# Kernel tuning notes

Measured on AMD Instinct MI355X. Metric: run time of the kernel, lower is better.

The kernel has to match this reference:

```python
import jax, jax.numpy as jnp
import numpy as np

B, S, IN_DIM, OUT_DIM = 16, 1024, 1024, 1024
NEG_SLOPE = 0.01  # torch F.leaky_relu default


def setup_inputs() -> dict:
    key = jax.random.key(0)
    ks = jax.random.split(key, 10)
    sc_in = 1.0 / np.sqrt(IN_DIM)
    sc_out = 1.0 / np.sqrt(OUT_DIM)
    return {
        "xs": jax.random.normal(ks[0], (B, S, IN_DIM), dtype=jnp.float32),
        "mask": jax.random.randint(ks[1], (B, S), 0, 2, dtype=jnp.int32),
        "Wk": jax.random.uniform(ks[2], (OUT_DIM, IN_DIM), jnp.float32, -sc_in, sc_in),
        "bk": jax.random.uniform(ks[3], (OUT_DIM,), jnp.float32, -sc_in, sc_in),
        "Wq": jax.random.uniform(ks[4], (OUT_DIM, IN_DIM), jnp.float32, -sc_in, sc_in),
        "bq": jax.random.uniform(ks[5], (OUT_DIM,), jnp.float32, -sc_in, sc_in),
        "Wv": jax.random.uniform(ks[6], (OUT_DIM, IN_DIM), jnp.float32, -sc_in, sc_in),
        "bv": jax.random.uniform(ks[7], (OUT_DIM,), jnp.float32, -sc_in, sc_in),
        "Wlin": jax.random.uniform(ks[8], (OUT_DIM, OUT_DIM), jnp.float32, -sc_out, sc_out),
        "blin": jax.random.uniform(ks[9], (OUT_DIM,), jnp.float32, -sc_out, sc_out),
    }


def reference(xs, mask, Wk, bk, Wq, bq, Wv, bv, Wlin, blin):
    # projections: torch Linear is x @ W.T + b
    K = jnp.einsum('bsi,oi->bso', xs, Wk) + bk  # [B,S,D]
    Q = jnp.einsum('bsi,oi->bso', xs, Wq) + bq  # [B,S,D]
    V = jnp.einsum('bsi,oi->bso', xs, Wv) + bv  # [B,S,D]
    # qk[b,s,e] = sum_d K[b,s,d] * Q[b,e,d]
    qk = jnp.einsum('bsd,bed->bse', K, Q) / xs.shape[-1]
    # mask.repeat(1,S).view(B,S,S) => element [b,i,j] = mask[b,j] (column/key mask)
    qk = jnp.where(mask[:, None, :].astype(bool), qk, -jnp.inf)
    a = jax.nn.softmax(qk, axis=-1)  # [B,S,S]
    # faithful to einsum('bij,bik->bik'): sum a over last axis, scale V elementwise
    attn = jnp.sum(a, axis=-1, keepdims=True) * V  # [B,S,D]
    out = jnp.einsum('bsd,od->bso', attn, Wlin) + blin
    return jnp.where(out >= 0, out, NEG_SLOPE * out)
```

## Files before the change

kernel.cpp:

```cpp
#include <hip/hip_runtime.h>
#include <hip/hip_bf16.h>
#include <stdint.h>


#define M_TOT 16384
#define KDIM  1024
#define NDIM  1024
#define NT    32

typedef __attribute__((ext_vector_type(8))) short bf16x8;
typedef __attribute__((ext_vector_type(4))) float f32x4;
typedef __attribute__((ext_vector_type(4))) unsigned short u16x4;
typedef __attribute__((ext_vector_type(8))) unsigned short u16x8;

static __device__ __forceinline__ unsigned short f2bf(float f) {
    union { float f; unsigned int u; } v; v.f = f;
    unsigned int u = v.u;
    return (unsigned short)((u + 0x7fffu + ((u >> 16) & 1u)) >> 16);
}

static __device__ __forceinline__ void gload16(const void* g, void* l) {
    __builtin_amdgcn_global_load_lds(
        (__attribute__((address_space(1))) void*)(g),
        (__attribute__((address_space(3))) void*)(l), 16, 0, 0);
}

static __device__ __forceinline__ int swz(int p) {
    return p ^ (((p >> 9) & 1) << 5) ^ (((p >> 8) & 1) << 4);
}

__global__ __launch_bounds__(256) void prep_kernel(
    const float* __restrict__ xs, const float* __restrict__ Wv,
    const float* __restrict__ bv, const float* __restrict__ Wlin,
    const float* __restrict__ blin, unsigned short* __restrict__ Wc,
    float* __restrict__ bcomb, unsigned short* __restrict__ Xb) {
    __shared__ unsigned short Al[64 * 32];
    __shared__ unsigned short Bl[64 * 32];
    const int bid = blockIdx.x;
    const int t = threadIdx.x;

    if (bid < 256) {
        const int ot = bid >> 4;
        const int it = bid & 15;
        const int w = t >> 6, l = t & 63;
        const int wr = (w >> 1) * 32, wc = (w & 1) * 32;
        const int lr = l & 15, lk = l >> 4;

        f32x4 acc[2][2] = {};

        for (int kt = 0; kt < KDIM / 32; ++kt) {
            float4 av[2];
            #pragma unroll
            for (int j = 0; j < 2; ++j) {
                const int row = j * 32 + (t >> 3);
                const int kq = t & 7;
                av[j] = *(const float4*)&Wlin[(ot * 64 + row) * KDIM + kt * 32 + kq * 4];
            }
            float4 bvv[2];
            #pragma unroll
            for (int j = 0; j < 2; ++j) {
                const int d = j * 16 + (t >> 4);
                const int i4 = t & 15;
                bvv[j] = *(const float4*)&Wv[(kt * 32 + d) * NDIM + it * 64 + i4 * 4];
            }
            __syncthreads();
            #pragma unroll
            for (int j = 0; j < 2; ++j) {
                const int row = j * 32 + (t >> 3);
                const int kq = t & 7;
                u16x4 p = { f2bf(av[j].x), f2bf(av[j].y), f2bf(av[j].z), f2bf(av[j].w) };
                *(u16x4*)&Al[row * 32 + kq * 4] = p;
            }
            #pragma unroll
            for (int j = 0; j < 2; ++j) {
                const int d = j * 16 + (t >> 4);
                const int i4 = t & 15;
                Bl[(i4 * 4 + 0) * 32 + d] = f2bf(bvv[j].x);
                Bl[(i4 * 4 + 1) * 32 + d] = f2bf(bvv[j].y);
                Bl[(i4 * 4 + 2) * 32 + d] = f2bf(bvv[j].z);
                Bl[(i4 * 4 + 3) * 32 + d] = f2bf(bvv[j].w);
            }
            __syncthreads();
            bf16x8 af[2], bfr[2];
            #pragma unroll
            for (int fi = 0; fi < 2; ++fi)
                af[fi] = *(bf16x8*)&Al[(wr + fi * 16 + lr) * 32 + lk * 8];
            #pragma unroll
            for (int fj = 0; fj < 2; ++fj)
                bfr[fj] = *(bf16x8*)&Bl[(wc + fj * 16 + lr) * 32 + lk * 8];
            #pragma unroll
            for (int fi = 0; fi < 2; ++fi)
                #pragma unroll
                for (int fj = 0; fj < 2; ++fj)
                    acc[fi][fj] = __builtin_amdgcn_mfma_f32_16x16x32_bf16(
                        af[fi], bfr[fj], acc[fi][fj], 0, 0, 0);
            __syncthreads();
        }
        #pragma unroll
        for (int fi = 0; fi < 2; ++fi)
            #pragma unroll
            for (int fj = 0; fj < 2; ++fj)
                #pragma unroll
                for (int r = 0; r < 4; ++r) {
                    const int o = ot * 64 + wr + fi * 16 + lk * 4 + r;
                    const int i = it * 64 + wc + fj * 16 + lr;
                    Wc[o * KDIM + i] = f2bf(acc[fi][fj][r]);
                }
    } else if (bid < 512) {
        const int wave = t >> 6, lane = t & 63;
        const int o = (bid - 256) * 4 + wave;
        float s = 0.f;
        for (int d = lane; d < KDIM; d += 64) s += Wlin[o * KDIM + d] * bv[d];
        #pragma unroll
        for (int off = 32; off > 0; off >>= 1) s += __shfl_down(s, off, 64);
        if (lane == 0) bcomb[o] = s + blin[o];
    } else {
        const int cb = bid - 512;
        const size_t base = ((size_t)cb * 256 + t) * 8;
        #pragma unroll
        for (int itr = 0; itr < 4; ++itr) {
            const size_t idx = base + (size_t)itr * (size_t)(2048 * 256 * 8);
            float4 a = *(const float4*)&xs[idx];
            float4 b = *(const float4*)&xs[idx + 4];
            u16x8 p = { f2bf(a.x), f2bf(a.y), f2bf(a.z), f2bf(a.w),
                        f2bf(b.x), f2bf(b.y), f2bf(b.z), f2bf(b.w) };
            *(u16x8*)&Xb[idx] = p;
        }
    }
}

__global__ __launch_bounds__(512, 2) void main_gemm_8p(
    const unsigned short* __restrict__ Xb, const unsigned short* __restrict__ Wc,
    const float* __restrict__ bcomb, float* __restrict__ out) {
    extern __shared__ char lds[];
    const int tid = threadIdx.x;
    const int w = tid >> 6, l = tid & 63;
    const int wm = w >> 2, wn = w & 3;
    const int lr = l & 15, lk = l >> 4;

    const int swzb = ((blockIdx.x & 7) << 5) + (blockIdx.x >> 3);
    const int mt = swzb >> 2, nt = swzb & 3;

    int aoff[8], boff[4];
    #pragma unroll
    for (int fi = 0; fi < 8; ++fi)
        aoff[fi] = swz((wm * 128 + fi * 16 + lr) * 64 + lk * 16);
    #pragma unroll
    for (int fj = 0; fj < 4; ++fj)
        boff[fj] = 16384 + swz((wn * 64 + fj * 16 + lr) * 64 + lk * 16);

    const char* srcA0; const char* srcA1; const char* srcB0; const char* srcB1;
    {
        int q0 = 0 * 8192 + w * 1024 + l * 16, p0 = swz(q0);
        int q1 = 1 * 8192 + w * 1024 + l * 16, p1 = swz(q1);
        srcA0 = (const char*)Xb + ((size_t)(mt * 256 + (p0 >> 6)) * KDIM) * 2 + (p0 & 63);
        srcA1 = (const char*)Xb + ((size_t)(mt * 256 + (p1 >> 6)) * KDIM) * 2 + (p1 & 63);
        srcB0 = (const char*)Wc + ((size_t)(nt * 256 + (p0 >> 6)) * KDIM) * 2 + (p0 & 63);
        srcB1 = (const char*)Wc + ((size_t)(nt * 256 + (p1 >> 6)) * KDIM) * 2 + (p1 & 63);
    }
    const int ldsw = w * 1024;

    f32x4 acc[8][4] = {};

    #pragma unroll
    for (int pt = 0; pt < 3; ++pt) {
        char* bb = lds + pt * 32768;
        gload16(srcA0 + (size_t)pt * 64, bb + ldsw);
        gload16(srcA1 + (size_t)pt * 64, bb + 8192 + ldsw);
        gload16(srcB0 + (size_t)pt * 64, bb + 16384 + ldsw);
        gload16(srcB1 + (size_t)pt * 64, bb + 24576 + ldsw);
    }

#define KTILE(T, STAGE_EN)                                                     \
    do {                                                                       \
        const char* bufp = lds + (size_t)((T) & 3) * 32768;                    \
        char* nb = lds + (size_t)(((T) + 3) & 3) * 32768;                      \
               \
        if (STAGE_EN) {                                                        \
            gload16(srcA0 + (size_t)((T) + 3) * 64, nb + ldsw);                \
            gload16(srcA1 + (size_t)((T) + 3) * 64, nb + 8192 + ldsw);         \
        }                                                                      \
        bf16x8 bfr[4], afr[4];                                                 \
        _Pragma("unroll")                                                      \
        for (int fj = 0; fj < 4; ++fj)                                         \
            bfr[fj] = *(const bf16x8*)(bufp + boff[fj]);                       \
        _Pragma("unroll")                                                      \
        for (int fi = 0; fi < 4; ++fi)                                         \
            afr[fi] = *(const bf16x8*)(bufp + aoff[fi]);                       \
        __builtin_amdgcn_s_barrier();                                          \
        __builtin_amdgcn_s_setprio(1);                                         \
        _Pragma("unroll")                                                      \
        for (int fi = 0; fi < 4; ++fi)                                         \
            _Pragma("unroll")                                                  \
            for (int fj = 0; fj < 4; ++fj)                                     \
                acc[fi][fj] = __builtin_amdgcn_mfma_f32_16x16x32_bf16(         \
                    afr[fi], bfr[fj], acc[fi][fj], 0, 0, 0);                   \
        __builtin_amdgcn_s_setprio(0);                                         \
        __builtin_amdgcn_s_barrier();                                          \
                        \
        if (STAGE_EN) {                                                        \
            gload16(srcB0 + (size_t)((T) + 3) * 64, nb + 16384 + ldsw);        \
            gload16(srcB1 + (size_t)((T) + 3) * 64, nb + 24576 + ldsw);        \
        }                                                                      \
        bf16x8 af2[4];                                                         \
        _Pragma("unroll")                                                      \
        for (int fi = 0; fi < 4; ++fi)                                         \
            af2[fi] = *(const bf16x8*)(bufp + aoff[4 + fi]);                   \
        __builtin_amdgcn_s_barrier();                                          \
        __builtin_amdgcn_s_setprio(1);                                         \
        _Pragma("unroll")                                                      \
        for (int fi = 0; fi < 4; ++fi)                                         \
            _Pragma("unroll")                                                  \
            for (int fj = 0; fj < 4; ++fj)                                     \
                acc[4 + fi][fj] = __builtin_amdgcn_mfma_f32_16x16x32_bf16(     \
                    af2[fi], bfr[fj], acc[4 + fi][fj], 0, 0, 0);               \
        __builtin_amdgcn_s_setprio(0);                                         \
    } while (0)

    for (int t = 0; t < NT - 3; ++t) {
        asm volatile("s_waitcnt vmcnt(8)" ::: "memory");
        __builtin_amdgcn_s_barrier();
        KTILE(t, 1);
    }
    asm volatile("s_waitcnt vmcnt(8)" ::: "memory");
    __builtin_amdgcn_s_barrier();
    KTILE(29, 0);
    asm volatile("s_waitcnt vmcnt(4)" ::: "memory");
    __builtin_amdgcn_s_barrier();
    KTILE(30, 0);
    asm volatile("s_waitcnt vmcnt(0)" ::: "memory");
    __builtin_amdgcn_s_barrier();
    KTILE(31, 0);
#undef KTILE

    #pragma unroll
    for (int fi = 0; fi < 8; ++fi)
        #pragma unroll
        for (int fj = 0; fj < 4; ++fj) {
            const int col = nt * 256 + wn * 64 + fj * 16 + lr;
            const float b = bcomb[col];
            #pragma unroll
            for (int r = 0; r < 4; ++r) {
                const int row = mt * 256 + wm * 128 + fi * 16 + lk * 4 + r;
                float v = acc[fi][fj][r] + b;
                out[(size_t)row * NDIM + col] = v >= 0.f ? v : 0.01f * v;
            }
        }
}

__global__ __launch_bounds__(256) void main_gemm_f32(
    const float* __restrict__ X, const unsigned short* __restrict__ Wc,
    const float* __restrict__ bcomb, float* __restrict__ out) {
    __shared__ unsigned short As[128 * 32];
    __shared__ unsigned short Bs[128 * 32];
    const int t = threadIdx.x;
    const int nt = blockIdx.x & 7;
    const int mt = blockIdx.x >> 3;
    const int w = t >> 6, l = t & 63;
    const int wr = (w >> 1) * 64, wcc = (w & 1) * 64;
    const int lr = l & 15, lk = l >> 4;

    f32x4 acc[4][4] = {};

    const int arow = t >> 3;
    const int akq = t & 7;
    const int brow = t >> 2;
    const int bc4 = t & 3;

    for (int kt = 0; kt < KDIM / 32; ++kt) {
        float4 av[4];
        #pragma unroll
        for (int j = 0; j < 4; ++j) {
            const int row = j * 32 + arow;
            av[j] = *(const float4*)&X[(mt * 128 + row) * KDIM + kt * 32 + akq * 4];
        }
        __syncthreads();
        #pragma unroll
        for (int j = 0; j < 4; ++j) {
            const int row = j * 32 + arow;
            u16x4 p = { f2bf(av[j].x), f2bf(av[j].y), f2bf(av[j].z), f2bf(av[j].w) };
            *(u16x4*)&As[row * 32 + akq * 4] = p;
        }
        #pragma unroll
        for (int j = 0; j < 2; ++j) {
            const int row = j * 64 + brow;
            const unsigned short* g = &Wc[(nt * 128 + row) * KDIM + kt * 32 + bc4 * 8];
            unsigned short* ldst = &Bs[(j * 256 + w * 64) * 8];
            gload16(g, ldst);
        }
        __syncthreads();
        bf16x8 af[4], bfr[4];
        #pragma unroll
        for (int fi = 0; fi < 4; ++fi)
            af[fi] = *(bf16x8*)&As[(wr + fi * 16 + lr) * 32 + lk * 8];
        #pragma unroll
        for (int fj = 0; fj < 4; ++fj)
            bfr[fj] = *(bf16x8*)&Bs[(wcc + fj * 16 + lr) * 32 + lk * 8];
        #pragma unroll
        for (int fi = 0; fi < 4; ++fi)
            #pragma unroll
            for (int fj = 0; fj < 4; ++fj)
                acc[fi][fj] = __builtin_amdgcn_mfma_f32_16x16x32_bf16(
                    af[fi], bfr[fj], acc[fi][fj], 0, 0, 0);
    }

    #pragma unroll
    for (int fi = 0; fi < 4; ++fi)
        #pragma unroll
        for (int fj = 0; fj < 4; ++fj) {
            const int col = nt * 128 + wcc + fj * 16 + lr;
            const float b = bcomb[col];
            #pragma unroll
            for (int r = 0; r < 4; ++r) {
                const int row = mt * 128 + wr + fi * 16 + lk * 4 + r;
                float v = acc[fi][fj][r] + b;
                out[row * NDIM + col] = v >= 0.f ? v : 0.01f * v;
            }
        }
}

extern "C" void kernel_launch(void* const* d_in, const int* in_sizes, int n_in,
                              void* d_out, int out_size, void* d_ws, size_t ws_size,
                              hipStream_t stream) {
    const float* xs   = (const float*)d_in[0];
    const float* Wv   = (const float*)d_in[6];
    const float* bv   = (const float*)d_in[7];
    const float* Wlin = (const float*)d_in[8];
    const float* blin = (const float*)d_in[9];

    unsigned short* Wc = (unsigned short*)d_ws;
    float* bcomb = (float*)((char*)d_ws + 2097152);
    unsigned short* Xb = (unsigned short*)((char*)d_ws + 2101248);
    float* out = (float*)d_out;

    const size_t NEED = 2101248 + (size_t)M_TOT * KDIM * 2;
    if (ws_size >= NEED) {
        (void)hipFuncSetAttribute((const void*)main_gemm_8p,
                                  hipFuncAttributeMaxDynamicSharedMemorySize,
                                  131072);
        hipLaunchKernelGGL(prep_kernel, dim3(512 + 2048), dim3(256), 0, stream,
                           xs, Wv, bv, Wlin, blin, Wc, bcomb, Xb);
        hipLaunchKernelGGL(main_gemm_8p, dim3(256), dim3(512), 131072, stream,
                           Xb, Wc, bcomb, out);
    } else {
        hipLaunchKernelGGL(prep_kernel, dim3(512), dim3(256), 0, stream,
                           xs, Wv, bv, Wlin, blin, Wc, bcomb, Xb);
        hipLaunchKernelGGL(main_gemm_f32, dim3((M_TOT / 128) * (NDIM / 128)),
                           dim3(256), 0, stream, xs, Wc, bcomb, out);
    }
}
```

Measured before the change: 86.14 us.

## Split weight-fusion prep into bf16 convert/transpose pass and tiled MFMA GEMM

The Wlin·Wv combined-weight computation moves from a 256-block kernel that converted fp32 to bf16 inside its k-loop into two stages. The first kernel transposes Wv and converts Wv and Wlin to bf16 scratch buffers placed in the output buffer. The second runs a 64-block 128x128 MFMA GEMM using direct global-to-LDS loads, alongside the xs conversion blocks. This targets the long serial prep GEMM that held up the main kernel, at the cost of an extra launch and reusing the output buffer as scratch.

```diff
diff --git a/kernel.cpp b/kernel.cpp
--- a/kernel.cpp
+++ b/kernel.cpp
@@ -29,94 +29,75 @@
     return p ^ (((p >> 9) & 1) << 5) ^ (((p >> 8) & 1) << 4);
 }
 
-__global__ __launch_bounds__(256) void prep_kernel(
-    const float* __restrict__ xs, const float* __restrict__ Wv,
-    const float* __restrict__ bv, const float* __restrict__ Wlin,
-    const float* __restrict__ blin, unsigned short* __restrict__ Wc,
-    float* __restrict__ bcomb, unsigned short* __restrict__ Xb) {
-    __shared__ unsigned short Al[64 * 32];
-    __shared__ unsigned short Bl[64 * 32];
+__global__ __launch_bounds__(256) void prep0_kernel(
+    const float* __restrict__ Wv, const float* __restrict__ Wlin,
+    const float* __restrict__ bv, const float* __restrict__ blin,
+    unsigned short* __restrict__ Wvt, unsigned short* __restrict__ Wlb,
+    float* __restrict__ bcomb) {
+    __shared__ float Tl[64 * 65];
     const int bid = blockIdx.x;
     const int t = threadIdx.x;
 
     if (bid < 256) {
-        const int ot = bid >> 4;
+        const int dt = bid >> 4;
         const int it = bid & 15;
-        const int w = t >> 6, l = t & 63;
-        const int wr = (w >> 1) * 32, wc = (w & 1) * 32;
-        const int lr = l & 15, lk = l >> 4;
-
-        f32x4 acc[2][2] = {};
-
-        for (int kt = 0; kt < KDIM / 32; ++kt) {
-            float4 av[2];
-            #pragma unroll
-            for (int j = 0; j < 2; ++j) {
-                const int row = j * 32 + (t >> 3);
-                const int kq = t & 7;
-                av[j] = *(const float4*)&Wlin[(ot * 64 + row) * KDIM + kt * 32 + kq * 4];
-            }
-            float4 bvv[2];
-            #pragma unroll
-            for (int j = 0; j < 2; ++j) {
-                const int d = j * 16 + (t >> 4);
-                const int i4 = t & 15;
-                bvv[j] = *(const float4*)&Wv[(kt * 32 + d) * NDIM + it * 64 + i4 * 4];
-            }
-            __syncthreads();
-            #pragma unroll
-            for (int j = 0; j < 2; ++j) {
-                const int row = j * 32 + (t >> 3);
-                const int kq = t & 7;
-                u16x4 p = { f2bf(av[j].x), f2bf(av[j].y), f2bf(av[j].z), f2bf(av[j].w) };
-                *(u16x4*)&Al[row * 32 + kq * 4] = p;
-            }
-            #pragma unroll
-            for (int j = 0; j < 2; ++j) {
-                const int d = j * 16 + (t >> 4);
-                const int i4 = t & 15;
-                Bl[(i4 * 4 + 0) * 32 + d] = f2bf(bvv[j].x);
-                Bl[(i4 * 4 + 1) * 32 + d] = f2bf(bvv[j].y);
-                Bl[(i4 * 4 + 2) * 32 + d] = f2bf(bvv[j].z);
-                Bl[(i4 * 4 + 3) * 32 + d] = f2bf(bvv[j].w);
-            }
-            __syncthreads();
-            bf16x8 af[2], bfr[2];
-            #pragma unroll
-            for (int fi = 0; fi < 2; ++fi)
-                af[fi] = *(bf16x8*)&Al[(wr + fi * 16 + lr) * 32 + lk * 8];
-            #pragma unroll
-            for (int fj = 0; fj < 2; ++fj)
-                bfr[fj] = *(bf16x8*)&Bl[(wc + fj * 16 + lr) * 32 + lk * 8];
-            #pragma unroll
-            for (int fi = 0; fi < 2; ++fi)
-                #pragma unroll
-                for (int fj = 0; fj < 2; ++fj)
-                    acc[fi][fj] = __builtin_amdgcn_mfma_f32_16x16x32_bf16(
-                        af[fi], bfr[fj], acc[fi][fj], 0, 0, 0);
-            __syncthreads();
-        }
-        #pragma unroll
-        for (int fi = 0; fi < 2; ++fi)
-            #pragma unroll
-            for (int fj = 0; fj < 2; ++fj)
-                #pragma unroll
-                for (int r = 0; r < 4; ++r) {
-                    const int o = ot * 64 + wr + fi * 16 + lk * 4 + r;
-                    const int i = it * 64 + wc + fj * 16 + lr;
-                    Wc[o * KDIM + i] = f2bf(acc[fi][fj][r]);
-                }
+        const int r = t >> 2;
+        const int c0 = (t & 3) * 16;
+        #pragma unroll
+        for (int u = 0; u < 4; ++u) {
+            float4 v = *(const float4*)&Wv[((size_t)(dt * 64 + r)) * NDIM + it * 64 + c0 + 4 * u];
+            Tl[r * 65 + c0 + 4 * u + 0] = v.x;
+            Tl[r * 65 + c0 + 4 * u + 1] = v.y;
+            Tl[r * 65 + c0 + 4 * u + 2] = v.z;
+            Tl[r * 65 + c0 + 4 * u + 3] = v.w;
+        }
+        __syncthreads();
+        const int i = t >> 2;
+        const int dq = (t & 3) * 16;
+        float v[16];
+        #pragma unroll
+        for (int u = 0; u < 16; ++u) v[u] = Tl[(dq + u) * 65 + i];
+        u16x8 p0 = { f2bf(v[0]), f2bf(v[1]), f2bf(v[2]), f2bf(v[3]),
+                     f2bf(v[4]), f2bf(v[5]), f2bf(v[6]), f2bf(v[7]) };
+        u16x8 p1 = { f2bf(v[8]), f2bf(v[9]), f2bf(v[10]), f2bf(v[11]),
+                     f2bf(v[12]), f2bf(v[13]), f2bf(v[14]), f2bf(v[15]) };
+        unsigned short* dst = &Wvt[((size_t)(it * 64 + i)) * KDIM + dt * 64 + dq];
+        *(u16x8*)dst = p0;
+        *(u16x8*)(dst + 8) = p1;
     } else if (bid < 512) {
+        const size_t idx = (((size_t)(bid - 256)) * 256 + t) * 16;
+        float4 a = *(const float4*)&Wlin[idx];
+        float4 b = *(const float4*)&Wlin[idx + 4];
+        float4 c = *(const float4*)&Wlin[idx + 8];
+        float4 d = *(const float4*)&Wlin[idx + 12];
+        u16x8 p0 = { f2bf(a.x), f2bf(a.y), f2bf(a.z), f2bf(a.w),
+                     f2bf(b.x), f2bf(b.y), f2bf(b.z), f2bf(b.w) };
+        u16x8 p1 = { f2bf(c.x), f2bf(c.y), f2bf(c.z), f2bf(c.w),
+                     f2bf(d.x), f2bf(d.y), f2bf(d.z), f2bf(d.w) };
+        *(u16x8*)&Wlb[idx] = p0;
+        *(u16x8*)&Wlb[idx + 8] = p1;
+    } else {
         const int wave = t >> 6, lane = t & 63;
-        const int o = (bid - 256) * 4 + wave;
+        const int o = (bid - 512) * 4 + wave;
         float s = 0.f;
         for (int d = lane; d < KDIM; d += 64) s += Wlin[o * KDIM + d] * bv[d];
         #pragma unroll
         for (int off = 32; off > 0; off >>= 1) s += __shfl_down(s, off, 64);
         if (lane == 0) bcomb[o] = s + blin[o];
-    } else {
-        const int cb = bid - 512;
-        const size_t base = ((size_t)cb * 256 + t) * 8;
+    }
+}
+
+__global__ __launch_bounds__(256) void prep1_kernel(
+    const unsigned short* __restrict__ Wlb, const unsigned short* __restrict__ Wvt,
+    const float* __restrict__ xs, unsigned short* __restrict__ Wc,
+    unsigned short* __restrict__ Xb) {
+    __shared__ unsigned short As[128 * 32];
+    __shared__ unsigned short Bs[128 * 32];
+    const int bid = blockIdx.x;
+    const int t = threadIdx.x;
+
+    if (bid >= 64) {
+        const size_t base = (((size_t)(bid - 64)) * 256 + t) * 8;
         #pragma unroll
         for (int itr = 0; itr < 4; ++itr) {
             const size_t idx = base + (size_t)itr * (size_t)(2048 * 256 * 8);
@@ -126,7 +107,58 @@
                         f2bf(b.x), f2bf(b.y), f2bf(b.z), f2bf(b.w) };
             *(u16x8*)&Xb[idx] = p;
         }
-    }
+        return;
+    }
+
+    const int nt8 = bid & 7;
+    const int mt8 = bid >> 3;
+    const int w = t >> 6, l = t & 63;
+    const int wr = (w >> 1) * 64, wcc = (w & 1) * 64;
+    const int lr = l & 15, lk = l >> 4;
+
+    f32x4 acc[4][4] = {};
+
+    const int srow = t >> 2;
+    const int sc8 = (t & 3) * 8;
+    const unsigned short* gA = &Wlb[((size_t)(mt8 * 128) + srow) * KDIM + sc8];
+    const unsigned short* gB = &Wvt[((size_t)(nt8 * 128) + srow) * KDIM + sc8];
+    unsigned short* lA0 = &As[w * 512];
+    unsigned short* lB0 = &Bs[w * 512];
+
+    for (int kt = 0; kt < KDIM / 32; ++kt) {
+        #pragma unroll
+        for (int j = 0; j < 2; ++j) {
+            gload16(gA + (size_t)j * 64 * KDIM + kt * 32, lA0 + j * 2048);
+            gload16(gB + (size_t)j * 64 * KDIM + kt * 32, lB0 + j * 2048);
+        }
+        __syncthreads();
+        bf16x8 af[4], bfr[4];
+        #pragma unroll
+        for (int fi = 0; fi < 4; ++fi)
+            af[fi] = *(bf16x8*)&As[(wr + fi * 16 + lr) * 32 + lk * 8];
+        #pragma unroll
+        for (int fj = 0; fj < 4; ++fj)
+            bfr[fj] = *(bf16x8*)&Bs[(wcc + fj * 16 + lr) * 32 + lk * 8];
+        #pragma unroll
+        for (int fi = 0; fi < 4; ++fi)
+            #pragma unroll
+            for (int fj = 0; fj < 4; ++fj)
+                acc[fi][fj] = __builtin_amdgcn_mfma_f32_16x16x32_bf16(
+                    af[fi], bfr[fj], acc[fi][fj], 0, 0, 0);
+        __syncthreads();
+    }
+
+    #pragma unroll
+    for (int fi = 0; fi < 4; ++fi)
+        #pragma unroll
+        for (int fj = 0; fj < 4; ++fj) {
+            const int col = nt8 * 128 + wcc + fj * 16 + lr;
+            #pragma unroll
+            for (int r = 0; r < 4; ++r) {
+                const int row = mt8 * 128 + wr + fi * 16 + lk * 4 + r;
+                Wc[(size_t)row * KDIM + col] = f2bf(acc[fi][fj][r]);
+            }
+        }
 }
 
 __global__ __launch_bounds__(512, 2) void main_gemm_8p(
@@ -175,7 +207,6 @@
     do {                                                                       \
         const char* bufp = lds + (size_t)((T) & 3) * 32768;                    \
         char* nb = lds + (size_t)(((T) + 3) & 3) * 32768;                      \
-               \
         if (STAGE_EN) {                                                        \
             gload16(srcA0 + (size_t)((T) + 3) * 64, nb + ldsw);                \
             gload16(srcA1 + (size_t)((T) + 3) * 64, nb + 8192 + ldsw);         \
@@ -197,7 +228,6 @@
                     afr[fi], bfr[fj], acc[fi][fj], 0, 0, 0);                   \
         __builtin_amdgcn_s_setprio(0);                                         \
         __builtin_amdgcn_s_barrier();                                          \
-                        \
         if (STAGE_EN) {                                                        \
             gload16(srcB0 + (size_t)((T) + 3) * 64, nb + 16384 + ldsw);        \
             gload16(srcB1 + (size_t)((T) + 3) * 64, nb + 24576 + ldsw);        \
@@ -333,18 +363,25 @@
     unsigned short* Xb = (unsigned short*)((char*)d_ws + 2101248);
     float* out = (float*)d_out;
 
+    unsigned short* Wvt = (unsigned short*)d_out;
+    unsigned short* Wlb = (unsigned short*)((char*)d_out + 2097152);
+
     const size_t NEED = 2101248 + (size_t)M_TOT * KDIM * 2;
     if (ws_size >= NEED) {
         (void)hipFuncSetAttribute((const void*)main_gemm_8p,
                                   hipFuncAttributeMaxDynamicSharedMemorySize,
                                   131072);
-        hipLaunchKernelGGL(prep_kernel, dim3(512 + 2048), dim3(256), 0, stream,
-                           xs, Wv, bv, Wlin, blin, Wc, bcomb, Xb);
+        hipLaunchKernelGGL(prep0_kernel, dim3(768), dim3(256), 0, stream,
+                           Wv, Wlin, bv, blin, Wvt, Wlb, bcomb);
+        hipLaunchKernelGGL(prep1_kernel, dim3(64 + 2048), dim3(256), 0, stream,
+                           Wlb, Wvt, xs, Wc, Xb);
         hipLaunchKernelGGL(main_gemm_8p, dim3(256), dim3(512), 131072, stream,
                            Xb, Wc, bcomb, out);
     } else {
-        hipLaunchKernelGGL(prep_kernel, dim3(512), dim3(256), 0, stream,
-                           xs, Wv, bv, Wlin, blin, Wc, bcomb, Xb);
+        hipLaunchKernelGGL(prep0_kernel, dim3(768), dim3(256), 0, stream,
+                           Wv, Wlin, bv, blin, Wvt, Wlb, bcomb);
+        hipLaunchKernelGGL(prep1_kernel, dim3(64), dim3(256), 0, stream,
+                           Wlb, Wvt, xs, Wc, Xb);
         hipLaunchKernelGGL(main_gemm_f32, dim3((M_TOT / 128) * (NDIM / 128)),
                            dim3(256), 0, stream, xs, Wc, bcomb, out);
     }
```

Result: faster. 83.10 us (-3.5%).
